# Performance work log

Measured on AMD Instinct MI355X. Metric: run time of the kernel, lower is better.

Reference implementation:

```python
import jax, jax.numpy as jnp
import numpy as np


def setup_inputs() -> dict:
    key = jax.random.key(0)
    k1, k2, k3, k4 = jax.random.split(key, 4)
    B, IN, OUT, R = 4096, 4096, 4096, 256
    x = jax.random.normal(k1, (B, IN), dtype=jnp.float32)
    U = jax.random.normal(k2, (R, IN), dtype=jnp.float32) / np.sqrt(IN)
    V = jax.random.normal(k3, (OUT, R), dtype=jnp.float32) / np.sqrt(R)
    bias = jax.random.uniform(k4, (OUT,), dtype=jnp.float32,
                              minval=-IN ** -0.5, maxval=IN ** -0.5)
    return {"x": x, "U": U, "V": V, "bias": bias}


def reference(x, U, V, bias):
    # Low-rank linear: out[b,j] = sum_k V[j,k] * (sum_i U[k,i] * x[b,i]) + bias[j]
    # (the torch loops with sparsity=1.0 / keep_stride==1 compute exactly this)
    t = jnp.einsum('bi,ri->br', x, U)        # [B, R]
    out = jnp.einsum('br,or->bo', t, V) + bias  # [B, OUT]
    return out
```

## Files before the change

### kernel.cpp

```cpp
#include <hip/hip_runtime.h>

typedef __attribute__((ext_vector_type(8))) short bf16x8;
typedef __attribute__((ext_vector_type(4))) float f32x4;

__device__ __forceinline__ unsigned short f2bf(float f) {
  unsigned int u = __float_as_uint(f);
  return (unsigned short)((u + 0x7fffu + ((u >> 16) & 1u)) >> 16);
}

__device__ __forceinline__ float bf2f(unsigned short s) {
  return __uint_as_float(((unsigned int)s) << 16);
}

__device__ __forceinline__ void gload_lds16(const void* g, void* l) {
  __builtin_amdgcn_global_load_lds((const __attribute__((address_space(1))) void*)g,
                                   (__attribute__((address_space(3))) void*)l,
                                   16, 0, 0);
}

__global__ void castUV(const float4* __restrict__ U, const float4* __restrict__ V,
                       ushort4* __restrict__ Ub, ushort4* __restrict__ Vb) {
  const int NU = 256 * 4096 / 4;
  int i = blockIdx.x * 256 + threadIdx.x;
  const float4* s; ushort4* d; int j;
  if (i < NU) { s = U; d = Ub; j = i; }
  else        { s = V; d = Vb; j = i - NU; }
  float4 v = s[j];
  ushort4 o;
  o.x = f2bf(v.x); o.y = f2bf(v.y); o.z = f2bf(v.z); o.w = f2bf(v.w);
  d[j] = o;
}

template <int MREP, int NREP, bool BIAS, bool AFP32, bool OUT_BF16>
__global__ __launch_bounds__(256)
void gemm_nt(const void* __restrict__ Ap,
             const unsigned short* __restrict__ B,
             const float* __restrict__ bias,
             void* __restrict__ Cv,
             int lda, int ldb, int ldc,
             int nkt, int kChunk, long long splitStride) {
  constexpr int BM = 32 * MREP;
  constexpr int BN = 32 * NREP;
  constexpr int AELT = AFP32 ? 4 : 2;
  constexpr int ISS_B = BN / 64;

  __shared__ __align__(16) char sA[2][BM * 32 * AELT];
  __shared__ unsigned short sB[2][BN * 32];

  const int tid = threadIdx.x;
  const int l = tid & 63;
  const int w = tid >> 6;
  const int wm = (w >> 1) * (MREP * 16);
  const int wn = (w & 1) * (NREP * 16);
  const int rm = blockIdx.x * BM;
  const int rn = blockIdx.y * BN;
  const int k0base = blockIdx.z * kChunk;

  const int lr = l & 15;
  const int lc8 = (l >> 4) * 8;

  auto stage = [&](int kt, int buf) {
    const int k0 = k0base + kt * 32;
#pragma unroll
    for (int is = 0; is < ISS_B; ++is) {
      int eo = is * 2048 + tid * 8;
      gload_lds16(B + (long long)(rn + (eo >> 5)) * ldb + k0 + (eo & 31),
                  &sB[buf][eo]);
    }
    if constexpr (AFP32) {
      const float* A32 = (const float*)Ap;
#pragma unroll
      for (int is = 0; is < BM * 32 / 1024; ++is) {
        int fo = is * 1024 + tid * 4;
        gload_lds16(A32 + (long long)(rm + (fo >> 5)) * lda + k0 + (fo & 31),
                    (float*)sA[buf] + fo);
      }
    } else {
      const unsigned short* A = (const unsigned short*)Ap;
#pragma unroll
      for (int is = 0; is < BM / 64; ++is) {
        int eo = is * 2048 + tid * 8;
        gload_lds16(A + (long long)(rm + (eo >> 5)) * lda + k0 + (eo & 31),
                    (unsigned short*)sA[buf] + eo);
      }
    }
  };

  f32x4 acc[MREP][NREP] = {};

  stage(0, 0);
  for (int kt = 0; kt < nkt; ++kt) {
    __syncthreads();
    if (kt + 1 < nkt) stage(kt + 1, (kt + 1) & 1);
    bf16x8 af[MREP], bfr[NREP];
    if constexpr (AFP32) {
      const float* a0 = (const float*)sA[kt & 1];
#pragma unroll
      for (int m = 0; m < MREP; ++m) {
        const float* p = a0 + (wm + m * 16 + lr) * 32 + lc8;
        float4 u0 = *(const float4*)p;
        float4 u1 = *(const float4*)(p + 4);
        bf16x8 t;
        t[0] = (short)f2bf(u0.x); t[1] = (short)f2bf(u0.y);
        t[2] = (short)f2bf(u0.z); t[3] = (short)f2bf(u0.w);
        t[4] = (short)f2bf(u1.x); t[5] = (short)f2bf(u1.y);
        t[6] = (short)f2bf(u1.z); t[7] = (short)f2bf(u1.w);
        af[m] = t;
      }
    } else {
      const unsigned short* a0 = (const unsigned short*)sA[kt & 1];
#pragma unroll
      for (int m = 0; m < MREP; ++m)
        af[m] = *(const bf16x8*)&a0[(wm + m * 16 + lr) * 32 + lc8];
    }
#pragma unroll
    for (int n = 0; n < NREP; ++n)
      bfr[n] = *(const bf16x8*)&sB[kt & 1][(wn + n * 16 + lr) * 32 + lc8];
#pragma unroll
    for (int m = 0; m < MREP; ++m)
#pragma unroll
      for (int n = 0; n < NREP; ++n)
        acc[m][n] = __builtin_amdgcn_mfma_f32_16x16x32_bf16(af[m], bfr[n], acc[m][n], 0, 0, 0);
  }

  const int r0 = rm + wm + (l >> 4) * 4;
  const int c0 = rn + wn + lr;
  if constexpr (OUT_BF16) {
    unsigned short* Cb = (unsigned short*)Cv + (long long)blockIdx.z * splitStride;
#pragma unroll
    for (int n = 0; n < NREP; ++n) {
      const int cc = c0 + n * 16;
#pragma unroll
      for (int m = 0; m < MREP; ++m)
#pragma unroll
        for (int i = 0; i < 4; ++i)
          Cb[(long long)(r0 + m * 16 + i) * ldc + cc] = f2bf(acc[m][n][i]);
    }
  } else {
    float* Cb = (float*)Cv + (long long)blockIdx.z * splitStride;
#pragma unroll
    for (int n = 0; n < NREP; ++n) {
      const int cc = c0 + n * 16;
      const float badd = BIAS ? bias[cc] : 0.0f;
#pragma unroll
      for (int m = 0; m < MREP; ++m)
#pragma unroll
        for (int i = 0; i < 4; ++i)
          Cb[(long long)(r0 + m * 16 + i) * ldc + cc] = acc[m][n][i] + badd;
    }
  }
}

__global__ void reduce16(const ushort4* __restrict__ P, ushort4* __restrict__ t) {
  const int S = 4096 * 256 / 4;
  int i = blockIdx.x * 256 + threadIdx.x;
  float sx = 0, sy = 0, sz = 0, sw = 0;
#pragma unroll
  for (int z = 0; z < 16; ++z) {
    ushort4 v = P[i + z * S];
    sx += bf2f(v.x); sy += bf2f(v.y); sz += bf2f(v.z); sw += bf2f(v.w);
  }
  ushort4 o;
  o.x = f2bf(sx); o.y = f2bf(sy); o.z = f2bf(sz); o.w = f2bf(sw);
  t[i] = o;
}

extern "C" void kernel_launch(void* const* d_in, const int* in_sizes, int n_in,
                              void* d_out, int out_size, void* d_ws, size_t ws_size,
                              hipStream_t stream) {
  const float* x    = (const float*)d_in[0];
  const float* U    = (const float*)d_in[1];
  const float* V    = (const float*)d_in[2];
  const float* bias = (const float*)d_in[3];
  float* out = (float*)d_out;

  char* ws = (char*)d_ws;
  unsigned short* P   = (unsigned short*)ws;
  unsigned short* tb  = (unsigned short*)(ws + (32u << 20));
  unsigned short* Ub  = (unsigned short*)(ws + (34u << 20));
  unsigned short* Vb  = (unsigned short*)(ws + (36u << 20));

  castUV<<<2048, 256, 0, stream>>>((const float4*)U, (const float4*)V,
                                   (ushort4*)Ub, (ushort4*)Vb);

  dim3 g1(4096 / 64, 1, 16);
  gemm_nt<2, 8, false, true, true><<<g1, 256, 0, stream>>>(
      x, Ub, nullptr, P, 4096, 4096, 256,
      8, 256, (long long)4096 * 256);

  reduce16<<<(4096 * 256 / 4) / 256, 256, 0, stream>>>((const ushort4*)P, (ushort4*)tb);

  dim3 g2(4096 / 128, 4096 / 128, 1);
  gemm_nt<4, 4, true, false, false><<<g2, 256, 0, stream>>>(
      tb, Vb, bias, out, 256, 256, 4096,
      8, 0, 0);
}
```

Before: 63.94 us.

## Keep U slice resident in LDS and stream x directly into registers for first GEMM

The first GEMM is restructured. Each block loads a pre-packed 256x256 bf16 slice of U into LDS once, in MFMA fragment order, and streams x rows from global memory straight into registers with double buffering. This removes the per-k-step LDS staging of fp32 x and the repeated B-tile loads and barriers. The prep kernel now writes U in a fragment-packed layout. The grid shrinks to 256 blocks of one block per CU with a large register footprint, which may limit latency hiding.

Result: faster. 58.87 us (-7.9%).

```diff
diff --git a/kernel.cpp b/kernel.cpp
--- a/kernel.cpp
+++ b/kernel.cpp
@@ -18,137 +18,95 @@
                                    16, 0, 0);
 }
 
-__global__ void castUV(const float4* __restrict__ U, const float4* __restrict__ V,
-                       ushort4* __restrict__ Ub, ushort4* __restrict__ Vb) {
-  const int NU = 256 * 4096 / 4;
+__global__ void prep(const float* __restrict__ U, const float4* __restrict__ V,
+                     unsigned short* __restrict__ Upk, ushort4* __restrict__ Vb) {
   int i = blockIdx.x * 256 + threadIdx.x;
-  const float4* s; ushort4* d; int j;
-  if (i < NU) { s = U; d = Ub; j = i; }
-  else        { s = V; d = Vb; j = i - NU; }
-  float4 v = s[j];
-  ushort4 o;
-  o.x = f2bf(v.x); o.y = f2bf(v.y); o.z = f2bf(v.z); o.w = f2bf(v.w);
-  d[j] = o;
-}
-
-template <int MREP, int NREP, bool BIAS, bool AFP32, bool OUT_BF16>
-__global__ __launch_bounds__(256)
-void gemm_nt(const void* __restrict__ Ap,
-             const unsigned short* __restrict__ B,
-             const float* __restrict__ bias,
-             void* __restrict__ Cv,
-             int lda, int ldb, int ldc,
-             int nkt, int kChunk, long long splitStride) {
-  constexpr int BM = 32 * MREP;
-  constexpr int BN = 32 * NREP;
-  constexpr int AELT = AFP32 ? 4 : 2;
-  constexpr int ISS_B = BN / 64;
-
-  __shared__ __align__(16) char sA[2][BM * 32 * AELT];
-  __shared__ unsigned short sB[2][BN * 32];
+  const int NUP = 128 * 16 * 64;
+  if (i < NUP) {
+    int l = i & 63, n = (i >> 6) & 15, jg = i >> 10;
+    const float* src = U + (long long)(n * 16 + (l & 15)) * 4096 + jg * 32 + (l >> 4) * 8;
+    float4 a = *(const float4*)src;
+    float4 b = *(const float4*)(src + 4);
+    ushort4 o0, o1;
+    o0.x = f2bf(a.x); o0.y = f2bf(a.y); o0.z = f2bf(a.z); o0.w = f2bf(a.w);
+    o1.x = f2bf(b.x); o1.y = f2bf(b.y); o1.z = f2bf(b.z); o1.w = f2bf(b.w);
+    ushort4* d = (ushort4*)(Upk + (long long)i * 8);
+    d[0] = o0; d[1] = o1;
+  } else {
+    int j = i - NUP;
+    float4 v = V[j];
+    ushort4 o;
+    o.x = f2bf(v.x); o.y = f2bf(v.y); o.z = f2bf(v.z); o.w = f2bf(v.w);
+    Vb[j] = o;
+  }
+}
+
+__global__ __launch_bounds__(256, 1)
+void gemm1_ures(const float* __restrict__ x, const unsigned short* __restrict__ Upk,
+                unsigned short* __restrict__ P) {
+  __shared__ unsigned short sU[8 * 16 * 64 * 8];
 
   const int tid = threadIdx.x;
   const int l = tid & 63;
   const int w = tid >> 6;
-  const int wm = (w >> 1) * (MREP * 16);
-  const int wn = (w & 1) * (NREP * 16);
-  const int rm = blockIdx.x * BM;
-  const int rn = blockIdx.y * BN;
-  const int k0base = blockIdx.z * kChunk;
-
+  const int mg = blockIdx.x;
+  const int z  = blockIdx.z;
   const int lr = l & 15;
-  const int lc8 = (l >> 4) * 8;
-
-  auto stage = [&](int kt, int buf) {
-    const int k0 = k0base + kt * 32;
-#pragma unroll
-    for (int is = 0; is < ISS_B; ++is) {
+  const int lg = l >> 4;
+
+  {
+    const unsigned short* src = Upk + (long long)z * 65536;
+#pragma unroll
+    for (int is = 0; is < 32; ++is) {
       int eo = is * 2048 + tid * 8;
-      gload_lds16(B + (long long)(rn + (eo >> 5)) * ldb + k0 + (eo & 31),
-                  &sB[buf][eo]);
-    }
-    if constexpr (AFP32) {
-      const float* A32 = (const float*)Ap;
-#pragma unroll
-      for (int is = 0; is < BM * 32 / 1024; ++is) {
-        int fo = is * 1024 + tid * 4;
-        gload_lds16(A32 + (long long)(rm + (fo >> 5)) * lda + k0 + (fo & 31),
-                    (float*)sA[buf] + fo);
+      gload_lds16(src + eo, &sU[eo]);
+    }
+  }
+
+  const float* xbase = x + (long long)(mg * 256 + w * 16 + lr) * 4096 + z * 256 + lg * 8;
+
+  float4 xr[2][8][2];
+#define XLOAD(p, s)                                                     \
+  {                                                                     \
+    const float* px_ = xbase + (long long)(p) * 64 * 4096;              \
+    _Pragma("unroll")                                                   \
+    for (int j_ = 0; j_ < 8; ++j_) {                                    \
+      xr[s][j_][0] = *(const float4*)(px_ + j_ * 32);                   \
+      xr[s][j_][1] = *(const float4*)(px_ + j_ * 32 + 4);               \
+    }                                                                   \
+  }
+
+  XLOAD(0, 0);
+  __syncthreads();
+
+  unsigned short* Pz = P + (long long)z * (4096LL * 256);
+
+#pragma unroll
+  for (int p = 0; p < 4; ++p) {
+    if (p < 3) XLOAD(p + 1, (p + 1) & 1);
+    f32x4 acc[16] = {};
+#pragma unroll
+    for (int j = 0; j < 8; ++j) {
+      float4 u0 = xr[p & 1][j][0], u1 = xr[p & 1][j][1];
+      bf16x8 af;
+      af[0] = (short)f2bf(u0.x); af[1] = (short)f2bf(u0.y);
+      af[2] = (short)f2bf(u0.z); af[3] = (short)f2bf(u0.w);
+      af[4] = (short)f2bf(u1.x); af[5] = (short)f2bf(u1.y);
+      af[6] = (short)f2bf(u1.z); af[7] = (short)f2bf(u1.w);
+#pragma unroll
+      for (int n = 0; n < 16; ++n) {
+        bf16x8 bfr = *(const bf16x8*)&sU[((j * 16 + n) * 64 + l) * 8];
+        acc[n] = __builtin_amdgcn_mfma_f32_16x16x32_bf16(af, bfr, acc[n], 0, 0, 0);
       }
-    } else {
-      const unsigned short* A = (const unsigned short*)Ap;
-#pragma unroll
-      for (int is = 0; is < BM / 64; ++is) {
-        int eo = is * 2048 + tid * 8;
-        gload_lds16(A + (long long)(rm + (eo >> 5)) * lda + k0 + (eo & 31),
-                    (unsigned short*)sA[buf] + eo);
-      }
-    }
-  };
-
-  f32x4 acc[MREP][NREP] = {};
-
-  stage(0, 0);
-  for (int kt = 0; kt < nkt; ++kt) {
-    __syncthreads();
-    if (kt + 1 < nkt) stage(kt + 1, (kt + 1) & 1);
-    bf16x8 af[MREP], bfr[NREP];
-    if constexpr (AFP32) {
-      const float* a0 = (const float*)sA[kt & 1];
-#pragma unroll
-      for (int m = 0; m < MREP; ++m) {
-        const float* p = a0 + (wm + m * 16 + lr) * 32 + lc8;
-        float4 u0 = *(const float4*)p;
-        float4 u1 = *(const float4*)(p + 4);
-        bf16x8 t;
-        t[0] = (short)f2bf(u0.x); t[1] = (short)f2bf(u0.y);
-        t[2] = (short)f2bf(u0.z); t[3] = (short)f2bf(u0.w);
-        t[4] = (short)f2bf(u1.x); t[5] = (short)f2bf(u1.y);
-        t[6] = (short)f2bf(u1.z); t[7] = (short)f2bf(u1.w);
-        af[m] = t;
-      }
-    } else {
-      const unsigned short* a0 = (const unsigned short*)sA[kt & 1];
-#pragma unroll
-      for (int m = 0; m < MREP; ++m)
-        af[m] = *(const bf16x8*)&a0[(wm + m * 16 + lr) * 32 + lc8];
-    }
-#pragma unroll
-    for (int n = 0; n < NREP; ++n)
-      bfr[n] = *(const bf16x8*)&sB[kt & 1][(wn + n * 16 + lr) * 32 + lc8];
-#pragma unroll
-    for (int m = 0; m < MREP; ++m)
-#pragma unroll
-      for (int n = 0; n < NREP; ++n)
-        acc[m][n] = __builtin_amdgcn_mfma_f32_16x16x32_bf16(af[m], bfr[n], acc[m][n], 0, 0, 0);
-  }
-
-  const int r0 = rm + wm + (l >> 4) * 4;
-  const int c0 = rn + wn + lr;
-  if constexpr (OUT_BF16) {
-    unsigned short* Cb = (unsigned short*)Cv + (long long)blockIdx.z * splitStride;
-#pragma unroll
-    for (int n = 0; n < NREP; ++n) {
-      const int cc = c0 + n * 16;
-#pragma unroll
-      for (int m = 0; m < MREP; ++m)
-#pragma unroll
-        for (int i = 0; i < 4; ++i)
-          Cb[(long long)(r0 + m * 16 + i) * ldc + cc] = f2bf(acc[m][n][i]);
-    }
-  } else {
-    float* Cb = (float*)Cv + (long long)blockIdx.z * splitStride;
-#pragma unroll
-    for (int n = 0; n < NREP; ++n) {
-      const int cc = c0 + n * 16;
-      const float badd = BIAS ? bias[cc] : 0.0f;
-#pragma unroll
-      for (int m = 0; m < MREP; ++m)
-#pragma unroll
-        for (int i = 0; i < 4; ++i)
-          Cb[(long long)(r0 + m * 16 + i) * ldc + cc] = acc[m][n][i] + badd;
-    }
-  }
+    }
+    const int r0 = mg * 256 + p * 64 + w * 16 + lg * 4;
+#pragma unroll
+    for (int n = 0; n < 16; ++n)
+#pragma unroll
+      for (int i2 = 0; i2 < 4; ++i2)
+        Pz[(long long)(r0 + i2) * 256 + n * 16 + lr] = f2bf(acc[n][i2]);
+  }
+#undef XLOAD
 }
 
 __global__ void reduce16(const ushort4* __restrict__ P, ushort4* __restrict__ t) {
@@ -163,6 +121,75 @@
   ushort4 o;
   o.x = f2bf(sx); o.y = f2bf(sy); o.z = f2bf(sz); o.w = f2bf(sw);
   t[i] = o;
+}
+
+__global__ __launch_bounds__(256)
+void gemm2(const unsigned short* __restrict__ A,
+           const unsigned short* __restrict__ B,
+           const float* __restrict__ bias,
+           float* __restrict__ C) {
+  constexpr int MREP = 4, NREP = 4;
+  __shared__ unsigned short sA[2][128 * 32];
+  __shared__ unsigned short sB[2][128 * 32];
+
+  const int tid = threadIdx.x;
+  const int l = tid & 63;
+  const int w = tid >> 6;
+  const int wm = (w >> 1) * 64;
+  const int wn = (w & 1) * 64;
+  const int rm = blockIdx.x * 128;
+  const int rn = blockIdx.y * 128;
+  const int lr = l & 15;
+  const int lc8 = (l >> 4) * 8;
+
+  auto stage = [&](int kt, int buf) {
+    const int k0 = kt * 32;
+#pragma unroll
+    for (int is = 0; is < 2; ++is) {
+      int eo = is * 2048 + tid * 8;
+      gload_lds16(B + (long long)(rn + (eo >> 5)) * 256 + k0 + (eo & 31), &sB[buf][eo]);
+    }
+#pragma unroll
+    for (int is = 0; is < 2; ++is) {
+      int eo = is * 2048 + tid * 8;
+      gload_lds16(A + (long long)(rm + (eo >> 5)) * 256 + k0 + (eo & 31), &sA[buf][eo]);
+    }
+  };
+
+  f32x4 acc[MREP][NREP] = {};
+
+  stage(0, 0);
+  for (int kt = 0; kt < 8; ++kt) {
+    __syncthreads();
+    if (kt + 1 < 8) stage(kt + 1, (kt + 1) & 1);
+    const unsigned short* a0 = sA[kt & 1];
+    const unsigned short* b0 = sB[kt & 1];
+    bf16x8 af[MREP], bfr[NREP];
+#pragma unroll
+    for (int m = 0; m < MREP; ++m)
+      af[m] = *(const bf16x8*)&a0[(wm + m * 16 + lr) * 32 + lc8];
+#pragma unroll
+    for (int n = 0; n < NREP; ++n)
+      bfr[n] = *(const bf16x8*)&b0[(wn + n * 16 + lr) * 32 + lc8];
+#pragma unroll
+    for (int m = 0; m < MREP; ++m)
+#pragma unroll
+      for (int n = 0; n < NREP; ++n)
+        acc[m][n] = __builtin_amdgcn_mfma_f32_16x16x32_bf16(af[m], bfr[n], acc[m][n], 0, 0, 0);
+  }
+
+  const int r0 = rm + wm + (l >> 4) * 4;
+  const int c0 = rn + wn + lr;
+#pragma unroll
+  for (int n = 0; n < NREP; ++n) {
+    const int cc = c0 + n * 16;
+    const float badd = bias[cc];
+#pragma unroll
+    for (int m = 0; m < MREP; ++m)
+#pragma unroll
+      for (int i = 0; i < 4; ++i)
+        C[(long long)(r0 + m * 16 + i) * 4096 + cc] = acc[m][n][i] + badd;
+  }
 }
 
 extern "C" void kernel_launch(void* const* d_in, const int* in_sizes, int n_in,
@@ -177,21 +204,16 @@
   char* ws = (char*)d_ws;
   unsigned short* P   = (unsigned short*)ws;
   unsigned short* tb  = (unsigned short*)(ws + (32u << 20));
-  unsigned short* Ub  = (unsigned short*)(ws + (34u << 20));
+  unsigned short* Upk = (unsigned short*)(ws + (34u << 20));
   unsigned short* Vb  = (unsigned short*)(ws + (36u << 20));
 
-  castUV<<<2048, 256, 0, stream>>>((const float4*)U, (const float4*)V,
-                                   (ushort4*)Ub, (ushort4*)Vb);
-
-  dim3 g1(4096 / 64, 1, 16);
-  gemm_nt<2, 8, false, true, true><<<g1, 256, 0, stream>>>(
-      x, Ub, nullptr, P, 4096, 4096, 256,
-      8, 256, (long long)4096 * 256);
+  prep<<<1536, 256, 0, stream>>>(U, (const float4*)V, Upk, (ushort4*)Vb);
+
+  dim3 g1(16, 1, 16);
+  gemm1_ures<<<g1, 256, 0, stream>>>(x, Upk, P);
 
   reduce16<<<(4096 * 256 / 4) / 256, 256, 0, stream>>>((const ushort4*)P, (ushort4*)tb);
 
-  dim3 g2(4096 / 128, 4096 / 128, 1);
-  gemm_nt<4, 4, true, false, false><<<g2, 256, 0, stream>>>(
-      tb, Vb, bias, out, 256, 256, 4096,
-      8, 0, 0);
-}
+  dim3 g2(32, 32, 1);
+  gemm2<<<g2, 256, 0, stream>>>(tb, Vb, bias, out);
+}
```
